# Optimization experiments

Measured on AMD Instinct MI355X. Metric: run time of the kernel, lower is better.

Reference implementation:

```python
import jax, jax.numpy as jnp
import numpy as np

B, C_IN, H, W = 4, 256, 48, 48
HEADS, HD = 8, 64
N = H * W
SCALE = 1.0 / (HD ** 0.5)


def setup_inputs() -> dict:
    key = jax.random.key(0)
    ks = jax.random.split(key, 5)
    x = jax.random.normal(ks[0], (B, C_IN, H, W), dtype=jnp.float32)
    # 1x1 conv weights, squeezed: [heads, head_channels, in_channels]
    Wq = jax.random.normal(ks[1], (HEADS, HD, C_IN), dtype=jnp.float32) * (C_IN ** -0.5)
    Wk = jax.random.normal(ks[2], (HEADS, HD, C_IN), dtype=jnp.float32) * (C_IN ** -0.5)
    Wv = jax.random.normal(ks[3], (HEADS, HD, C_IN), dtype=jnp.float32) * (C_IN ** -0.5)
    # output 1x1 conv: [in_channels, heads*head_channels]
    Wo = jax.random.normal(ks[4], (C_IN, HEADS * HD), dtype=jnp.float32) * ((HEADS * HD) ** -0.5)
    return {"x": x, "Wq": Wq, "Wk": Wk, "Wv": Wv, "Wo": Wo}


def reference(x, Wq, Wk, Wv, Wo):
    b, c, h, w = x.shape
    n = h * w
    xf = x.reshape(b, c, n)  # [B, C, N]
    # per-head 1x1 convs == batched projections -> [heads, B, N, HD]
    q = jnp.einsum('hdc,bcn->hbnd', Wq, xf)
    k = jnp.einsum('hdc,bcn->hbnd', Wk, xf)
    v = jnp.einsum('hdc,bcn->hbnd', Wv, xf)
    scores = jnp.einsum('hbnd,hbmd->hbnm', q, k) * SCALE  # [heads, B, N, N]
    probs = jax.nn.softmax(scores, axis=-1)
    ws = jnp.einsum('hbnm,hbmd->hbnd', probs, v)  # [heads, B, N, HD]
    # faithful replication of torch: transpose(1,2) then reshape(B, heads*HD, H, W)
    ws = jnp.transpose(ws, (0, 2, 1, 3))  # [heads, N, B, HD]
    ws = ws.reshape(b, HEADS * HD, h, w)
    out = jnp.einsum('oc,bchw->bohw', Wo, ws)  # output 1x1 conv
    return out
```

## Files before the change

kernel.cpp:

```cpp
#include <hip/hip_runtime.h>

#define B_     4
#define CIN    256
#define NTOK   2304
#define HEADS  8
#define HD     64
#define SCALE  0.125f
#define LOG2E  1.44269504088896f
#define QSCALE (SCALE * LOG2E)
#define PBIAS  4.0f
#define QKV_ELEMS (HEADS * B_ * NTOK * HD)
#define HBSTRIDE 147456
#define WSZ    131072

typedef _Float16 f16;
typedef _Float16 __attribute__((ext_vector_type(8))) h8v;
typedef _Float16 __attribute__((ext_vector_type(4))) h4v;
typedef ushort   __attribute__((ext_vector_type(8))) us8;
typedef float    __attribute__((ext_vector_type(16))) f16v;

__device__ inline uint pk2(float a, float b) {
    auto v = __builtin_amdgcn_cvt_pkrtz(a, b);
    return __builtin_bit_cast(uint, v);
}
#define EXP2(x) __builtin_amdgcn_exp2f(x)

#define GLOAD_LDS(g, l) __builtin_amdgcn_global_load_lds( \
    (const __attribute__((address_space(1))) unsigned int*)(g), \
    (__attribute__((address_space(3))) unsigned int*)(l), 16, 0, 0)

__global__ __launch_bounds__(256) void prep(
    const float* __restrict__ x,
    const float* __restrict__ Wq, const float* __restrict__ Wk,
    const float* __restrict__ Wv, const float* __restrict__ Wo,
    f16* __restrict__ wc, f16* __restrict__ woc, f16* __restrict__ xt)
{
    __shared__ float T[64][65];
    const int bid = blockIdx.x;
    const int tid = threadIdx.x;

    if (bid < 512) {
        int e4 = (bid * 256 + tid) * 4;
        const float* src; f16* dst; float mult = 1.0f; int off;
        if (e4 < WSZ)          { src = Wq; off = e4;           dst = wc;           mult = QSCALE; }
        else if (e4 < 2 * WSZ) { src = Wk; off = e4 - WSZ;     dst = wc + WSZ; }
        else if (e4 < 3 * WSZ) { src = Wv; off = e4 - 2 * WSZ; dst = wc + 2 * WSZ; }
        else                   { src = Wo; off = e4 - 3 * WSZ; dst = woc; }
        float4 r = *(const float4*)(src + off);
        h4v hv;
        hv.x = (f16)(r.x * mult); hv.y = (f16)(r.y * mult);
        hv.z = (f16)(r.z * mult); hv.w = (f16)(r.w * mult);
        *(h4v*)(dst + off) = hv;
        return;
    }

    const int r  = bid - 512;
    const int n0 = (r % 36) * 64;
    const int c0 = ((r / 36) % 4) * 64;
    const int b  = r / 144;
    const float* sb = x + ((size_t)b * CIN + c0) * NTOK;
    #pragma unroll
    for (int i = 0; i < 16; ++i) {
        int idx = tid + 256 * i;
        int rr = idx >> 6, ll = idx & 63;
        T[ll][rr] = sb[(size_t)rr * NTOK + n0 + ll];
    }
    __syncthreads();
    const size_t ob = ((size_t)b * NTOK + n0) * CIN + c0;
    #pragma unroll
    for (int i = 0; i < 4; ++i) {
        int idx = tid + 256 * i;
        int row = idx >> 4, c4 = (idx & 15) * 4;
        h4v v;
        v.x = (f16)T[row][c4 + 0]; v.y = (f16)T[row][c4 + 1];
        v.z = (f16)T[row][c4 + 2]; v.w = (f16)T[row][c4 + 3];
        *(h4v*)(xt + ob + (size_t)row * CIN + c4) = v;
    }
}

__global__ __launch_bounds__(128) void proj_mfma(
    const f16* __restrict__ wc, const f16* __restrict__ xt,
    f16* __restrict__ qh, f16* __restrict__ kh, f16* __restrict__ vth)
{
    const int ntile = blockIdx.x;
    const int hp    = blockIdx.y;
    const int b     = blockIdx.z;
    const int p     = hp >> 3, h = hp & 7;
    const int hb    = h * 4 + b;
    const f16* Wp = wc + ((size_t)p * 8 + h) * (HD * CIN);

    __shared__ __align__(16) f16 Ws[2][64][64], Xs[2][64][64];

    const int tid = threadIdx.x;
    const int w = tid >> 6, lane = tid & 63;
    const int lm = lane & 31, lh = lane >> 5;
    const int n_loc  = w * 32 + lm;
    const int n_glob = ntile * 64 + n_loc;

    const f16* xb = xt + ((size_t)b * NTOK + ntile * 64) * CIN;

    auto stage = [&](int buf, int c0) {
        const f16* src = (w == 0) ? Wp : xb;
        f16* dst = (w == 0) ? &Ws[buf][0][0] : &Xs[buf][0][0];
        #pragma unroll
        for (int i = 0; i < 8; ++i) {
            int g = i * 64 + lane; int row = g >> 3; int c = (g & 7) ^ (row & 7);
            GLOAD_LDS(src + (size_t)row * CIN + c0 + c * 8, dst + i * 512);
        }
    };

    f16v o0, o1;
    #pragma unroll
    for (int i = 0; i < 16; ++i) { o0[i] = 0.f; o1[i] = 0.f; }

    stage(0, 0);
    for (int c0 = 0; c0 < CIN; c0 += 64) {
        const int cur = (c0 >> 6) & 1;
        __syncthreads();
        if (c0 + 64 < CIN) stage(cur ^ 1, c0 + 64);
        #pragma unroll
        for (int s = 0; s < 4; ++s) {
            const int pp = ((2 * s + lh) ^ (lm & 7)) * 8;
            h8v a0 = *(const h8v*)&Ws[cur][lm][pp];
            h8v a1 = *(const h8v*)&Ws[cur][lm + 32][pp];
            h8v bh = *(const h8v*)&Xs[cur][n_loc][pp];
            o0 = __builtin_amdgcn_mfma_f32_32x32x16_f16(a0, bh, o0, 0, 0, 0);
            o1 = __builtin_amdgcn_mfma_f32_32x32x16_f16(a1, bh, o1, 0, 0, 0);
        }
    }

    const size_t hboff = (size_t)hb * HBSTRIDE;
    if (p < 2) {
        f16* oh = ((p == 0) ? qh : kh) + hboff + (size_t)n_glob * 64;
        #pragma unroll
        for (int t = 0; t < 2; ++t) {
            const f16v& oc = t ? o1 : o0;
            #pragma unroll
            for (int g = 0; g < 4; ++g) {
                int d0 = 8 * g + 4 * lh + 32 * t;
                h4v hv;
                hv.x = (f16)oc[4 * g + 0]; hv.y = (f16)oc[4 * g + 1];
                hv.z = (f16)oc[4 * g + 2]; hv.w = (f16)oc[4 * g + 3];
                *(h4v*)(oh + d0) = hv;
            }
        }
    } else {
        f16* oh = vth + hboff;
        #pragma unroll
        for (int t = 0; t < 2; ++t) {
            const f16v& oc = t ? o1 : o0;
            #pragma unroll
            for (int r = 0; r < 16; ++r) {
                int d = (r & 3) + 8 * (r >> 2) + 4 * lh + 32 * t;
                oh[(size_t)d * NTOK + n_glob] = (f16)oc[r];
            }
        }
    }
}

__global__ __launch_bounds__(256, 2) void attn_mfma(
    const f16* __restrict__ qh, const f16* __restrict__ kh,
    const f16* __restrict__ vth, f16* __restrict__ wsth)
{
    const int bid   = blockIdx.x;
    const int xcd   = bid & 7;
    const int slot  = bid >> 3;
    const int hb    = xcd * 4 + (slot / 18);
    const int rpair = slot % 18;
    const int h_    = hb >> 2, b = hb & 3;
    const int tid   = threadIdx.x;
    const int w     = tid >> 6;
    const int lane  = tid & 63;
    const int lm    = lane & 31;
    const int lh    = lane >> 5;
    const int qg    = w >> 1;
    const int ks    = w & 1;

    __shared__ __align__(16) f16 SMEM[2][2][64][64];
    __shared__ float LRED[256];

    const size_t hboff = (size_t)hb * HBSTRIDE;
    const int mA = rpair * 128 + qg * 64 + lm;
    const int mB = mA + 32;

    h8v QfA[4], QfB[4];
    #pragma unroll
    for (int s = 0; s < 4; ++s) {
        QfA[s] = *(const h8v*)(qh + hboff + (size_t)mA * 64 + (2 * s + lh) * 8);
        QfB[s] = *(const h8v*)(qh + hboff + (size_t)mB * 64 + (2 * s + lh) * 8);
    }

    f16v oA0, oA1, oB0, oB1;
    #pragma unroll
    for (int i = 0; i < 16; ++i) { oA0[i] = 0.f; oA1[i] = 0.f; oB0[i] = 0.f; oB1[i] = 0.f; }
    float lsumA = 0.f, lsumB = 0.f;

    const int  sv  = w >> 1;
    const int  stp = w & 1;
    const f16* gb  = (sv == 0) ? kh + hboff : vth + hboff;

    auto stage = [&](int st) {
        const int kts = 2 * st + stp;
        f16* dst = &SMEM[sv][stp][0][0];
        #pragma unroll
        for (int i = 0; i < 8; ++i) {
            int g   = i * 64 + lane;
            int row = g >> 3;
            int c   = (g & 7) ^ (row & 7);
            const f16* src = (sv == 0)
                ? gb + kts * 4096 + row * 64 + c * 8
                : gb + (size_t)row * 2304 + kts * 64 + c * 8;
            GLOAD_LDS(src, dst + i * 512);
        }
    };

    stage(0);
    __syncthreads();

    for (int st = 0; st < 18; ++st) {
        f16v sA0, sA1, sB0, sB1;
        #pragma unroll
        for (int i = 0; i < 16; ++i) {
            sA0[i] = -PBIAS; sA1[i] = -PBIAS; sB0[i] = -PBIAS; sB1[i] = -PBIAS;
        }

        __builtin_amdgcn_s_setprio(1);
        #pragma unroll
        for (int s = 0; s < 4; ++s) {
            const int p = ((2 * s + lh) ^ (lm & 7)) * 8;
            h8v k0 = *(const h8v*)&SMEM[0][ks][lm][p];
            h8v k1 = *(const h8v*)&SMEM[0][ks][lm + 32][p];
            sA0 = __builtin_amdgcn_mfma_f32_32x32x16_f16(k0, QfA[s], sA0, 0, 0, 0);
            sA1 = __builtin_amdgcn_mfma_f32_32x32x16_f16(k1, QfA[s], sA1, 0, 0, 0);
            sB0 = __builtin_amdgcn_mfma_f32_32x32x16_f16(k0, QfB[s], sB0, 0, 0, 0);
            sB1 = __builtin_amdgcn_mfma_f32_32x32x16_f16(k1, QfB[s], sB1, 0, 0, 0);
        }
        __builtin_amdgcn_s_setprio(0);

        __syncthreads();
        if (st + 1 < 18 && sv == 0) stage(st + 1);

        float pa0 = 0.f, pa1 = 0.f, pa2 = 0.f, pa3 = 0.f;
        float pb0 = 0.f, pb1 = 0.f, pb2 = 0.f, pb3 = 0.f;
        #pragma unroll
        for (int i = 0; i < 16; i += 4) {
            sA0[i+0] = EXP2(sA0[i+0]); pa0 += sA0[i+0];
            sA0[i+1] = EXP2(sA0[i+1]); pa1 += sA0[i+1];
            sA0[i+2] = EXP2(sA0[i+2]); pa2 += sA0[i+2];
            sA0[i+3] = EXP2(sA0[i+3]); pa3 += sA0[i+3];
        }
        #pragma unroll
        for (int i = 0; i < 16; i += 4) {
            sA1[i+0] = EXP2(sA1[i+0]); pa0 += sA1[i+0];
            sA1[i+1] = EXP2(sA1[i+1]); pa1 += sA1[i+1];
            sA1[i+2] = EXP2(sA1[i+2]); pa2 += sA1[i+2];
            sA1[i+3] = EXP2(sA1[i+3]); pa3 += sA1[i+3];
        }
        #pragma unroll
        for (int i = 0; i < 16; i += 4) {
            sB0[i+0] = EXP2(sB0[i+0]); pb0 += sB0[i+0];
            sB0[i+1] = EXP2(sB0[i+1]); pb1 += sB0[i+1];
            sB0[i+2] = EXP2(sB0[i+2]); pb2 += sB0[i+2];
            sB0[i+3] = EXP2(sB0[i+3]); pb3 += sB0[i+3];
        }
        #pragma unroll
        for (int i = 0; i < 16; i += 4) {
            sB1[i+0] = EXP2(sB1[i+0]); pb0 += sB1[i+0];
            sB1[i+1] = EXP2(sB1[i+1]); pb1 += sB1[i+1];
            sB1[i+2] = EXP2(sB1[i+2]); pb2 += sB1[i+2];
            sB1[i+3] = EXP2(sB1[i+3]); pb3 += sB1[i+3];
        }
        lsumA += (pa0 + pa1) + (pa2 + pa3);
        lsumB += (pb0 + pb1) + (pb2 + pb3);

        uint PpkA[2][8], PpkB[2][8];
        #pragma unroll
        for (int pr = 0; pr < 8; ++pr) {
            PpkA[0][pr] = pk2(sA0[2 * pr], sA0[2 * pr + 1]);
            PpkA[1][pr] = pk2(sA1[2 * pr], sA1[2 * pr + 1]);
            PpkB[0][pr] = pk2(sB0[2 * pr], sB0[2 * pr + 1]);
            PpkB[1][pr] = pk2(sB1[2 * pr], sB1[2 * pr + 1]);
        }

        h8v pfA[4], pfB[4];
        #pragma unroll
        for (int s = 0; s < 4; ++s) {
            const int jt = s >> 1, q = 4 * (s & 1);
            auto a02 = __builtin_amdgcn_permlane32_swap(
                PpkA[jt][q + 0], PpkA[jt][q + 2], false, false);
            auto a13 = __builtin_amdgcn_permlane32_swap(
                PpkA[jt][q + 1], PpkA[jt][q + 3], false, false);
            uint4 ua = { a02[0], a13[0], a02[1], a13[1] };
            pfA[s] = __builtin_bit_cast(h8v, ua);
            auto b02 = __builtin_amdgcn_permlane32_swap(
                PpkB[jt][q + 0], PpkB[jt][q + 2], false, false);
            auto b13 = __builtin_amdgcn_permlane32_swap(
                PpkB[jt][q + 1], PpkB[jt][q + 3], false, false);
            uint4 ub = { b02[0], b13[0], b02[1], b13[1] };
            pfB[s] = __builtin_bit_cast(h8v, ub);
        }

        __builtin_amdgcn_s_setprio(1);
        #pragma unroll
        for (int s = 0; s < 4; ++s) {
            const int p = ((2 * s + lh) ^ (lm & 7)) * 8;
            h8v v0 = *(const h8v*)&SMEM[1][ks][lm][p];
            h8v v1 = *(const h8v*)&SMEM[1][ks][lm + 32][p];
            oA0 = __builtin_amdgcn_mfma_f32_32x32x16_f16(v0, pfA[s], oA0, 0, 0, 0);
            oA1 = __builtin_amdgcn_mfma_f32_32x32x16_f16(v1, pfA[s], oA1, 0, 0, 0);
            oB0 = __builtin_amdgcn_mfma_f32_32x32x16_f16(v0, pfB[s], oB0, 0, 0, 0);
            oB1 = __builtin_amdgcn_mfma_f32_32x32x16_f16(v1, pfB[s], oB1, 0, 0, 0);
        }
        __builtin_amdgcn_s_setprio(0);

        __syncthreads();
        if (st + 1 < 18 && sv == 1) stage(st + 1);
    }

    float* red = (float*)&SMEM[0][0][0][0];
    if (ks == 1) {
        float* dA = red + (size_t)(qg * 128 + lane) * 32;
        float* dB = red + (size_t)(qg * 128 + 64 + lane) * 32;
        #pragma unroll
        for (int i = 0; i < 16; ++i) {
            dA[i] = oA0[i]; dA[16 + i] = oA1[i];
            dB[i] = oB0[i]; dB[16 + i] = oB1[i];
        }
        LRED[qg * 128 + lane] = lsumA;
        LRED[qg * 128 + 64 + lane] = lsumB;
    }
    __syncthreads();
    if (ks == 0) {
        const float* sA = red + (size_t)(qg * 128 + lane) * 32;
        const float* sB = red + (size_t)(qg * 128 + 64 + lane) * 32;
        #pragma unroll
        for (int i = 0; i < 16; ++i) {
            oA0[i] += sA[i]; oA1[i] += sA[16 + i];
            oB0[i] += sB[i]; oB1[i] += sB[16 + i];
        }
        lsumA += LRED[qg * 128 + lane];
        lsumB += LRED[qg * 128 + 64 + lane];
        lsumA += __shfl_xor(lsumA, 32);
        lsumB += __shfl_xor(lsumB, 32);
        float invA = 1.0f / lsumA, invB = 1.0f / lsumB;

        f16* wrA = wsth + ((size_t)h_ * NTOK + mA) * 256 + b * 64;
        f16* wrB = wsth + ((size_t)h_ * NTOK + mB) * 256 + b * 64;
        #pragma unroll
        for (int g = 0; g < 4; ++g) {
            h4v r0, r1;
            r0.x = (f16)(oA0[4 * g + 0] * invA); r0.y = (f16)(oA0[4 * g + 1] * invA);
            r0.z = (f16)(oA0[4 * g + 2] * invA); r0.w = (f16)(oA0[4 * g + 3] * invA);
            *(h4v*)(wrA + 8 * g + 4 * lh) = r0;
            r1.x = (f16)(oA1[4 * g + 0] * invA); r1.y = (f16)(oA1[4 * g + 1] * invA);
            r1.z = (f16)(oA1[4 * g + 2] * invA); r1.w = (f16)(oA1[4 * g + 3] * invA);
            *(h4v*)(wrA + 32 + 8 * g + 4 * lh) = r1;
        }
        #pragma unroll
        for (int g = 0; g < 4; ++g) {
            h4v r0, r1;
            r0.x = (f16)(oB0[4 * g + 0] * invB); r0.y = (f16)(oB0[4 * g + 1] * invB);
            r0.z = (f16)(oB0[4 * g + 2] * invB); r0.w = (f16)(oB0[4 * g + 3] * invB);
            *(h4v*)(wrB + 8 * g + 4 * lh) = r0;
            r1.x = (f16)(oB1[4 * g + 0] * invB); r1.y = (f16)(oB1[4 * g + 1] * invB);
            r1.z = (f16)(oB1[4 * g + 2] * invB); r1.w = (f16)(oB1[4 * g + 3] * invB);
            *(h4v*)(wrB + 32 + 8 * g + 4 * lh) = r1;
        }
    }
}

__global__ __launch_bounds__(128) void outconv_mfma(
    const f16* __restrict__ woc, const f16* __restrict__ ws,
    float* __restrict__ out)
{
    const int ntile = blockIdx.x;
    const int otile = blockIdx.y;
    const int b     = blockIdx.z;

    __shared__ __align__(16) f16 Wos[2][64][64];
    __shared__ __align__(16) f16 Xs[2][64][72];

    const int tid = threadIdx.x;
    const int w = tid >> 6, lane = tid & 63;
    const int lm = lane & 31, lh = lane >> 5;
    const int n_loc  = w * 32 + lm;
    const int n_glob = ntile * 64 + n_loc;
    const int pr = tid >> 2;
    const int qn = tid & 3;

    const f16* Wb = woc + (size_t)(otile * 64) * 512;
    const f16* wsb = ws + (size_t)b * 512 * NTOK + ntile * 64 + qn * 16;

    auto stageW = [&](int buf, int c0) {
        #pragma unroll
        for (int j = 0; j < 4; ++j) {
            int i = w * 4 + j;
            int g = i * 64 + lane; int row = g >> 3; int c = (g & 7) ^ (row & 7);
            GLOAD_LDS(Wb + (size_t)row * 512 + c0 + c * 8,
                      &Wos[buf][0][0] + i * 512);
        }
    };

    uint4 x0, x1, x2, x3;
    auto loadB = [&](int c0) {
        const f16* r0 = wsb + (size_t)(c0 + 2 * pr) * NTOK;
        const f16* r1 = r0 + NTOK;
        x0 = *(const uint4*)(r0);
        x1 = *(const uint4*)(r0 + 8);
        x2 = *(const uint4*)(r1);
        x3 = *(const uint4*)(r1 + 8);
    };
    auto storeB = [&](int buf) {
        us8 a0 = __builtin_bit_cast(us8, x0), a1 = __builtin_bit_cast(us8, x1);
        us8 b0 = __builtin_bit_cast(us8, x2), b1 = __builtin_bit_cast(us8, x3);
        #pragma unroll
        for (int j = 0; j < 8; ++j) {
            *(uint*)&Xs[buf][qn * 16 + j][2 * pr]     = (uint)a0[j] | ((uint)b0[j] << 16);
            *(uint*)&Xs[buf][qn * 16 + 8 + j][2 * pr] = (uint)a1[j] | ((uint)b1[j] << 16);
        }
    };

    f16v o0, o1;
    #pragma unroll
    for (int i = 0; i < 16; ++i) { o0[i] = 0.f; o1[i] = 0.f; }

    stageW(0, 0);
    loadB(0);
    storeB(0);
    for (int c0 = 0; c0 < 512; c0 += 64) {
        const int cur = (c0 >> 6) & 1;
        __syncthreads();
        if (c0 + 64 < 512) { stageW(cur ^ 1, c0 + 64); loadB(c0 + 64); }
        #pragma unroll
        for (int s = 0; s < 4; ++s) {
            const int pp = ((2 * s + lh) ^ (lm & 7)) * 8;
            const int co = (2 * s + lh) * 8;
            h8v a0 = *(const h8v*)&Wos[cur][lm][pp];
            h8v a1 = *(const h8v*)&Wos[cur][lm + 32][pp];
            h8v bh = *(const h8v*)&Xs[cur][n_loc][co];
            o0 = __builtin_amdgcn_mfma_f32_32x32x16_f16(a0, bh, o0, 0, 0, 0);
            o1 = __builtin_amdgcn_mfma_f32_32x32x16_f16(a1, bh, o1, 0, 0, 0);
        }
        if (c0 + 64 < 512) storeB(cur ^ 1);
    }

    #pragma unroll
    for (int t = 0; t < 2; ++t) {
        const f16v& oc = t ? o1 : o0;
        #pragma unroll
        for (int r = 0; r < 16; ++r) {
            int orow = otile * 64 + (r & 3) + 8 * (r >> 2) + 4 * lh + 32 * t;
            out[((size_t)b * CIN + orow) * NTOK + n_glob] = oc[r];
        }
    }
}

extern "C" void kernel_launch(void* const* d_in, const int* in_sizes, int n_in,
                              void* d_out, int out_size, void* d_ws, size_t ws_size,
                              hipStream_t stream)
{
    const float* x  = (const float*)d_in[0];
    const float* Wq = (const float*)d_in[1];
    const float* Wk = (const float*)d_in[2];
    const float* Wv = (const float*)d_in[3];
    const float* Wo = (const float*)d_in[4];
    float* out = (float*)d_out;

    f16* qh   = (f16*)d_ws;
    f16* kh   = qh   + QKV_ELEMS;
    f16* vth  = kh   + QKV_ELEMS;
    f16* wsth = vth  + QKV_ELEMS;
    f16* xt   = wsth;
    f16* wc   = wsth + QKV_ELEMS;
    f16* woc  = wc   + 3 * WSZ;

    prep<<<dim3(1088), 256, 0, stream>>>(x, Wq, Wk, Wv, Wo, wc, woc, xt);
    proj_mfma<<<dim3(36, 24, 4), 128, 0, stream>>>(wc, xt, qh, kh, vth);
    attn_mfma<<<dim3(576), 256, 0, stream>>>(qh, kh, vth, wsth);
    outconv_mfma<<<dim3(36, 4, 4), 128, 0, stream>>>(woc, wsth, out);
}
```

Baseline: 169.2 us.

## Software-pipeline attention loop with double-buffered K/V and one barrier per tile

Doubles the K/V shared-memory tiles and restructures the attention loop so the QK MFMAs for tile t are issued alongside the softmax and PV MFMAs for tile t-1, leaving one barrier per iteration instead of two. The aim is to overlap exp/pack work with matrix-core work and to hide K/V staging latency. Shared memory doubles and launch bounds drop to one block per SM, which lowers occupancy and puts more pressure on registers. The reduction buffer is padded to stride 33 and also carries the row sums, removing the separate LRED array.

```diff
diff --git a/kernel.cpp b/kernel.cpp
--- a/kernel.cpp
+++ b/kernel.cpp
@@ -158,7 +158,7 @@
     }
 }
 
-__global__ __launch_bounds__(256, 2) void attn_mfma(
+__global__ __launch_bounds__(256, 1) void attn_mfma(
     const f16* __restrict__ qh, const f16* __restrict__ kh,
     const f16* __restrict__ vth, f16* __restrict__ wsth)
 {
@@ -176,8 +176,7 @@
     const int qg    = w >> 1;
     const int ks    = w & 1;
 
-    __shared__ __align__(16) f16 SMEM[2][2][64][64];
-    __shared__ float LRED[256];
+    __shared__ __align__(16) f16 SMEM[2][2][2][64][64];
 
     const size_t hboff = (size_t)hb * HBSTRIDE;
     const int mA = rpair * 128 + qg * 64 + lm;
@@ -191,17 +190,19 @@
     }
 
     f16v oA0, oA1, oB0, oB1;
+    f16v sA0, sA1, sB0, sB1;
     #pragma unroll
     for (int i = 0; i < 16; ++i) { oA0[i] = 0.f; oA1[i] = 0.f; oB0[i] = 0.f; oB1[i] = 0.f; }
     float lsumA = 0.f, lsumB = 0.f;
+    h8v pfA[4], pfB[4];
 
     const int  sv  = w >> 1;
     const int  stp = w & 1;
     const f16* gb  = (sv == 0) ? kh + hboff : vth + hboff;
 
-    auto stage = [&](int st) {
-        const int kts = 2 * st + stp;
-        f16* dst = &SMEM[sv][stp][0][0];
+    auto stage = [&](int tb, int ti) {
+        const int kts = 2 * ti + stp;
+        f16* dst = &SMEM[sv][tb][stp][0][0];
         #pragma unroll
         for (int i = 0; i < 8; ++i) {
             int g   = i * 64 + lane;
@@ -214,32 +215,24 @@
         }
     };
 
-    stage(0);
-    __syncthreads();
-
-    for (int st = 0; st < 18; ++st) {
-        f16v sA0, sA1, sB0, sB1;
+    auto DO_QK = [&](int tb) {
         #pragma unroll
         for (int i = 0; i < 16; ++i) {
             sA0[i] = -PBIAS; sA1[i] = -PBIAS; sB0[i] = -PBIAS; sB1[i] = -PBIAS;
         }
-
-        __builtin_amdgcn_s_setprio(1);
         #pragma unroll
         for (int s = 0; s < 4; ++s) {
             const int p = ((2 * s + lh) ^ (lm & 7)) * 8;
-            h8v k0 = *(const h8v*)&SMEM[0][ks][lm][p];
-            h8v k1 = *(const h8v*)&SMEM[0][ks][lm + 32][p];
+            h8v k0 = *(const h8v*)&SMEM[0][tb][ks][lm][p];
+            h8v k1 = *(const h8v*)&SMEM[0][tb][ks][lm + 32][p];
             sA0 = __builtin_amdgcn_mfma_f32_32x32x16_f16(k0, QfA[s], sA0, 0, 0, 0);
             sA1 = __builtin_amdgcn_mfma_f32_32x32x16_f16(k1, QfA[s], sA1, 0, 0, 0);
             sB0 = __builtin_amdgcn_mfma_f32_32x32x16_f16(k0, QfB[s], sB0, 0, 0, 0);
             sB1 = __builtin_amdgcn_mfma_f32_32x32x16_f16(k1, QfB[s], sB1, 0, 0, 0);
         }
-        __builtin_amdgcn_s_setprio(0);
-
-        __syncthreads();
-        if (st + 1 < 18 && sv == 0) stage(st + 1);
-
+    };
+
+    auto DO_SM = [&]() {
         float pa0 = 0.f, pa1 = 0.f, pa2 = 0.f, pa3 = 0.f;
         float pb0 = 0.f, pb1 = 0.f, pb2 = 0.f, pb3 = 0.f;
         #pragma unroll
@@ -273,73 +266,91 @@
         lsumA += (pa0 + pa1) + (pa2 + pa3);
         lsumB += (pb0 + pb1) + (pb2 + pb3);
 
-        uint PpkA[2][8], PpkB[2][8];
-        #pragma unroll
-        for (int pr = 0; pr < 8; ++pr) {
-            PpkA[0][pr] = pk2(sA0[2 * pr], sA0[2 * pr + 1]);
-            PpkA[1][pr] = pk2(sA1[2 * pr], sA1[2 * pr + 1]);
-            PpkB[0][pr] = pk2(sB0[2 * pr], sB0[2 * pr + 1]);
-            PpkB[1][pr] = pk2(sB1[2 * pr], sB1[2 * pr + 1]);
-        }
-
-        h8v pfA[4], pfB[4];
         #pragma unroll
         for (int s = 0; s < 4; ++s) {
-            const int jt = s >> 1, q = 4 * (s & 1);
-            auto a02 = __builtin_amdgcn_permlane32_swap(
-                PpkA[jt][q + 0], PpkA[jt][q + 2], false, false);
-            auto a13 = __builtin_amdgcn_permlane32_swap(
-                PpkA[jt][q + 1], PpkA[jt][q + 3], false, false);
+            const int q2 = 8 * (s & 1);
+            const f16v& ja = (s >> 1) ? sA1 : sA0;
+            const f16v& jb = (s >> 1) ? sB1 : sB0;
+            uint a0 = pk2(ja[q2 + 0], ja[q2 + 1]);
+            uint a1 = pk2(ja[q2 + 2], ja[q2 + 3]);
+            uint a2 = pk2(ja[q2 + 4], ja[q2 + 5]);
+            uint a3 = pk2(ja[q2 + 6], ja[q2 + 7]);
+            auto a02 = __builtin_amdgcn_permlane32_swap(a0, a2, false, false);
+            auto a13 = __builtin_amdgcn_permlane32_swap(a1, a3, false, false);
             uint4 ua = { a02[0], a13[0], a02[1], a13[1] };
             pfA[s] = __builtin_bit_cast(h8v, ua);
-            auto b02 = __builtin_amdgcn_permlane32_swap(
-                PpkB[jt][q + 0], PpkB[jt][q + 2], false, false);
-            auto b13 = __builtin_amdgcn_permlane32_swap(
-                PpkB[jt][q + 1], PpkB[jt][q + 3], false, false);
+            uint b0 = pk2(jb[q2 + 0], jb[q2 + 1]);
+            uint b1 = pk2(jb[q2 + 2], jb[q2 + 3]);
+            uint b2 = pk2(jb[q2 + 4], jb[q2 + 5]);
+            uint b3 = pk2(jb[q2 + 6], jb[q2 + 7]);
+            auto b02 = __builtin_amdgcn_permlane32_swap(b0, b2, false, false);
+            auto b13 = __builtin_amdgcn_permlane32_swap(b1, b3, false, false);
             uint4 ub = { b02[0], b13[0], b02[1], b13[1] };
             pfB[s] = __builtin_bit_cast(h8v, ub);
         }
-
-        __builtin_amdgcn_s_setprio(1);
+    };
+
+    auto DO_PV = [&](int tb) {
         #pragma unroll
         for (int s = 0; s < 4; ++s) {
             const int p = ((2 * s + lh) ^ (lm & 7)) * 8;
-            h8v v0 = *(const h8v*)&SMEM[1][ks][lm][p];
-            h8v v1 = *(const h8v*)&SMEM[1][ks][lm + 32][p];
+            h8v v0 = *(const h8v*)&SMEM[1][tb][ks][lm][p];
+            h8v v1 = *(const h8v*)&SMEM[1][tb][ks][lm + 32][p];
             oA0 = __builtin_amdgcn_mfma_f32_32x32x16_f16(v0, pfA[s], oA0, 0, 0, 0);
             oA1 = __builtin_amdgcn_mfma_f32_32x32x16_f16(v1, pfA[s], oA1, 0, 0, 0);
             oB0 = __builtin_amdgcn_mfma_f32_32x32x16_f16(v0, pfB[s], oB0, 0, 0, 0);
             oB1 = __builtin_amdgcn_mfma_f32_32x32x16_f16(v1, pfB[s], oB1, 0, 0, 0);
         }
+    };
+
+    if (sv == 0) stage(0, 0);
+    __syncthreads();
+
+    stage(sv == 0 ? 1 : 0, sv == 0 ? 1 : 0);
+    __builtin_amdgcn_s_setprio(1);
+    DO_QK(0);
+    __builtin_amdgcn_s_setprio(0);
+    __syncthreads();
+
+    for (int t = 1; t < 18; ++t) {
+        if (sv == 0) { if (t < 17) stage((t + 1) & 1, t + 1); }
+        else         stage(t & 1, t);
+
+        DO_SM();
+        __builtin_amdgcn_s_setprio(1);
+        DO_PV((t - 1) & 1);
+        DO_QK(t & 1);
         __builtin_amdgcn_s_setprio(0);
-
         __syncthreads();
-        if (st + 1 < 18 && sv == 1) stage(st + 1);
-    }
-
-    float* red = (float*)&SMEM[0][0][0][0];
+    }
+
+    DO_SM();
+    __builtin_amdgcn_s_setprio(1);
+    DO_PV(1);
+    __builtin_amdgcn_s_setprio(0);
+    __syncthreads();
+
+    float* red = (float*)&SMEM[0][0][0][0][0];
     if (ks == 1) {
-        float* dA = red + (size_t)(qg * 128 + lane) * 32;
-        float* dB = red + (size_t)(qg * 128 + 64 + lane) * 32;
+        float* dA = red + (size_t)(qg * 128 + lane) * 33;
+        float* dB = red + (size_t)(qg * 128 + 64 + lane) * 33;
         #pragma unroll
         for (int i = 0; i < 16; ++i) {
             dA[i] = oA0[i]; dA[16 + i] = oA1[i];
             dB[i] = oB0[i]; dB[16 + i] = oB1[i];
         }
-        LRED[qg * 128 + lane] = lsumA;
-        LRED[qg * 128 + 64 + lane] = lsumB;
+        dA[32] = lsumA; dB[32] = lsumB;
     }
     __syncthreads();
     if (ks == 0) {
-        const float* sA = red + (size_t)(qg * 128 + lane) * 32;
-        const float* sB = red + (size_t)(qg * 128 + 64 + lane) * 32;
+        const float* sA = red + (size_t)(qg * 128 + lane) * 33;
+        const float* sB = red + (size_t)(qg * 128 + 64 + lane) * 33;
         #pragma unroll
         for (int i = 0; i < 16; ++i) {
             oA0[i] += sA[i]; oA1[i] += sA[16 + i];
             oB0[i] += sB[i]; oB1[i] += sB[16 + i];
         }
-        lsumA += LRED[qg * 128 + lane];
-        lsumB += LRED[qg * 128 + 64 + lane];
+        lsumA += sA[32]; lsumB += sB[32];
         lsumA += __shfl_xor(lsumA, 32);
         lsumB += __shfl_xor(lsumB, 32);
         float invA = 1.0f / lsumA, invB = 1.0f / lsumB;
```

Measured after the change: 193.6 us. +14.4%, slower.

## Fuse Q/K/V projections per block to reuse X tile, rotate LDS reduction layout

Applied to the files above, without the earlier changes.

The projection kernel now computes all three projections (Q, K, V) in a single block, so each staged X tile is reused across three weight tiles and the grid shrinks threefold. This cuts redundant global loads of X, at the cost of more LDS (three weight tiles per buffer), more accumulator registers (six MFMA accumulators), and fewer blocks in flight. Separately, the attention kernel's split-K reduction through shared memory now rotates each row's element index by the row number, spreading accesses across LDS banks to reduce conflicts on the strided float rows.

```diff
diff --git a/kernel.cpp b/kernel.cpp
--- a/kernel.cpp
+++ b/kernel.cpp
@@ -78,18 +78,17 @@
     }
 }
 
-__global__ __launch_bounds__(128) void proj_mfma(
+__global__ __launch_bounds__(128, 2) void proj_mfma(
     const f16* __restrict__ wc, const f16* __restrict__ xt,
     f16* __restrict__ qh, f16* __restrict__ kh, f16* __restrict__ vth)
 {
     const int ntile = blockIdx.x;
-    const int hp    = blockIdx.y;
+    const int h     = blockIdx.y;
     const int b     = blockIdx.z;
-    const int p     = hp >> 3, h = hp & 7;
     const int hb    = h * 4 + b;
-    const f16* Wp = wc + ((size_t)p * 8 + h) * (HD * CIN);
-
-    __shared__ __align__(16) f16 Ws[2][64][64], Xs[2][64][64];
+
+    __shared__ __align__(16) f16 Ws[2][3][64][64];
+    __shared__ __align__(16) f16 Xs[2][64][64];
 
     const int tid = threadIdx.x;
     const int w = tid >> 6, lane = tid & 63;
@@ -98,20 +97,36 @@
     const int n_glob = ntile * 64 + n_loc;
 
     const f16* xb = xt + ((size_t)b * NTOK + ntile * 64) * CIN;
+    const f16* Wh = wc + (size_t)h * (HD * CIN);
 
     auto stage = [&](int buf, int c0) {
-        const f16* src = (w == 0) ? Wp : xb;
-        f16* dst = (w == 0) ? &Ws[buf][0][0] : &Xs[buf][0][0];
-        #pragma unroll
-        for (int i = 0; i < 8; ++i) {
-            int g = i * 64 + lane; int row = g >> 3; int c = (g & 7) ^ (row & 7);
-            GLOAD_LDS(src + (size_t)row * CIN + c0 + c * 8, dst + i * 512);
+        #pragma unroll
+        for (int i = 0; i < 16; ++i) {
+            int j = i & 7;
+            int g = j * 64 + lane; int row = g >> 3; int c = (g & 7) ^ (row & 7);
+            const f16* src; f16* dst;
+            if (w == 0) {
+                int p = i >> 3;
+                src = Wh + (size_t)p * WSZ + (size_t)row * CIN + c0 + c * 8;
+                dst = &Ws[buf][p][0][0] + j * 512;
+            } else if (i < 8) {
+                src = Wh + (size_t)2 * WSZ + (size_t)row * CIN + c0 + c * 8;
+                dst = &Ws[buf][2][0][0] + j * 512;
+            } else {
+                src = xb + (size_t)row * CIN + c0 + c * 8;
+                dst = &Xs[buf][0][0] + j * 512;
+            }
+            GLOAD_LDS(src, dst);
         }
     };
 
-    f16v o0, o1;
-    #pragma unroll
-    for (int i = 0; i < 16; ++i) { o0[i] = 0.f; o1[i] = 0.f; }
+    f16v acc[3][2];
+    #pragma unroll
+    for (int p = 0; p < 3; ++p)
+        #pragma unroll
+        for (int t = 0; t < 2; ++t)
+            #pragma unroll
+            for (int i = 0; i < 16; ++i) acc[p][t][i] = 0.f;
 
     stage(0, 0);
     for (int c0 = 0; c0 < CIN; c0 += 64) {
@@ -121,20 +136,24 @@
         #pragma unroll
         for (int s = 0; s < 4; ++s) {
             const int pp = ((2 * s + lh) ^ (lm & 7)) * 8;
-            h8v a0 = *(const h8v*)&Ws[cur][lm][pp];
-            h8v a1 = *(const h8v*)&Ws[cur][lm + 32][pp];
             h8v bh = *(const h8v*)&Xs[cur][n_loc][pp];
-            o0 = __builtin_amdgcn_mfma_f32_32x32x16_f16(a0, bh, o0, 0, 0, 0);
-            o1 = __builtin_amdgcn_mfma_f32_32x32x16_f16(a1, bh, o1, 0, 0, 0);
+            #pragma unroll
+            for (int p = 0; p < 3; ++p) {
+                h8v a0 = *(const h8v*)&Ws[cur][p][lm][pp];
+                h8v a1 = *(const h8v*)&Ws[cur][p][lm + 32][pp];
+                acc[p][0] = __builtin_amdgcn_mfma_f32_32x32x16_f16(a0, bh, acc[p][0], 0, 0, 0);
+                acc[p][1] = __builtin_amdgcn_mfma_f32_32x32x16_f16(a1, bh, acc[p][1], 0, 0, 0);
+            }
         }
     }
 
     const size_t hboff = (size_t)hb * HBSTRIDE;
-    if (p < 2) {
+    #pragma unroll
+    for (int p = 0; p < 2; ++p) {
         f16* oh = ((p == 0) ? qh : kh) + hboff + (size_t)n_glob * 64;
         #pragma unroll
         for (int t = 0; t < 2; ++t) {
-            const f16v& oc = t ? o1 : o0;
+            const f16v& oc = acc[p][t];
             #pragma unroll
             for (int g = 0; g < 4; ++g) {
                 int d0 = 8 * g + 4 * lh + 32 * t;
@@ -144,11 +163,12 @@
                 *(h4v*)(oh + d0) = hv;
             }
         }
-    } else {
+    }
+    {
         f16* oh = vth + hboff;
         #pragma unroll
         for (int t = 0; t < 2; ++t) {
-            const f16v& oc = t ? o1 : o0;
+            const f16v& oc = acc[2][t];
             #pragma unroll
             for (int r = 0; r < 16; ++r) {
                 int d = (r & 3) + 8 * (r >> 2) + 4 * lh + 32 * t;
@@ -318,28 +338,30 @@
     }
 
     float* red = (float*)&SMEM[0][0][0][0];
+    const int rowA = qg * 128 + lane;
+    const int rowB = rowA + 64;
     if (ks == 1) {
-        float* dA = red + (size_t)(qg * 128 + lane) * 32;
-        float* dB = red + (size_t)(qg * 128 + 64 + lane) * 32;
+        float* dA = red + (size_t)rowA * 32;
+        float* dB = red + (size_t)rowB * 32;
         #pragma unroll
         for (int i = 0; i < 16; ++i) {
-            dA[i] = oA0[i]; dA[16 + i] = oA1[i];
-            dB[i] = oB0[i]; dB[16 + i] = oB1[i];
-        }
-        LRED[qg * 128 + lane] = lsumA;
-        LRED[qg * 128 + 64 + lane] = lsumB;
+            dA[(i + rowA) & 31] = oA0[i]; dA[(16 + i + rowA) & 31] = oA1[i];
+            dB[(i + rowB) & 31] = oB0[i]; dB[(16 + i + rowB) & 31] = oB1[i];
+        }
+        LRED[rowA] = lsumA;
+        LRED[rowB] = lsumB;
     }
     __syncthreads();
     if (ks == 0) {
-        const float* sA = red + (size_t)(qg * 128 + lane) * 32;
-        const float* sB = red + (size_t)(qg * 128 + 64 + lane) * 32;
+        const float* sA = red + (size_t)rowA * 32;
+        const float* sB = red + (size_t)rowB * 32;
         #pragma unroll
         for (int i = 0; i < 16; ++i) {
-            oA0[i] += sA[i]; oA1[i] += sA[16 + i];
-            oB0[i] += sB[i]; oB1[i] += sB[16 + i];
-        }
-        lsumA += LRED[qg * 128 + lane];
-        lsumB += LRED[qg * 128 + 64 + lane];
+            oA0[i] += sA[(i + rowA) & 31]; oA1[i] += sA[(16 + i + rowA) & 31];
+            oB0[i] += sB[(i + rowB) & 31]; oB1[i] += sB[(16 + i + rowB) & 31];
+        }
+        lsumA += LRED[rowA];
+        lsumB += LRED[rowB];
         lsumA += __shfl_xor(lsumA, 32);
         lsumB += __shfl_xor(lsumB, 32);
         float invA = 1.0f / lsumA, invB = 1.0f / lsumB;
@@ -475,7 +497,7 @@
     f16* woc  = wc   + 3 * WSZ;
 
     prep<<<dim3(1088), 256, 0, stream>>>(x, Wq, Wk, Wv, Wo, wc, woc, xt);
-    proj_mfma<<<dim3(36, 24, 4), 128, 0, stream>>>(wc, xt, qh, kh, vth);
+    proj_mfma<<<dim3(36, 8, 4), 128, 0, stream>>>(wc, xt, qh, kh, vth);
     attn_mfma<<<dim3(576), 256, 0, stream>>>(qh, kh, vth, wsth);
     outconv_mfma<<<dim3(36, 4, 4), 128, 0, stream>>>(woc, wsth, out);
 }
```

Result: slower. 176.3 us (+4.1%).
